# Kernel optimization log

Hardware: AMD Instinct MI355X
Metric: run time of the kernel (lower is better)

Reference implementation:

```python
import jax, jax.numpy as jnp
import numpy as np

HID = 512; NH = 8; HD = 64          # attention dims
SH = 8; SD = 32; SDIM = 256          # delta-state dims
NL = 6; FFN = 1536; VOC = 63
THETA = 500000.0; EPS = 1e-6


def rmsnorm(x, w, eps=EPS):
    xf = x.astype(jnp.float32)
    n = xf * jax.lax.rsqrt(jnp.mean(xf * xf, axis=-1, keepdims=True) + eps)
    return (n * w).astype(x.dtype)


def rotate_half(x):
    x1, x2 = jnp.split(x, 2, axis=-1)
    return jnp.concatenate([-x2, x1], axis=-1)


def delta_state(h, S0, Wk, Wv, Wq, Wbw, Wbb, Waw, Wab, Wout, nw, gw):
    # Gated delta-rule associative memory. h: (B,L,HID), S0: (B,SH,SD,SD)
    B, L, _ = h.shape
    k = (h @ Wk.T).reshape(B, L, SH, SD)
    v = (h @ Wv.T).reshape(B, L, SH, SD)
    q = (h @ Wq.T).reshape(B, L, SH, SD)
    beta = jax.nn.sigmoid(h @ Wbw.T + Wbb).reshape(B, L, SH, SD)
    alpha = jax.nn.sigmoid(h @ Waw.T + Wab).reshape(B, L, SH, SD)
    k = k / jnp.maximum(jnp.linalg.norm(k, axis=-1, keepdims=True), 1e-12)
    gate = h @ gw.T  # (B,L,SDIM)
    xs = tuple(jnp.moveaxis(a, 1, 0) for a in (k, v, q, beta, alpha))  # (L,B,SH,SD)

    def step(S, inp):
        k_t, v_t, q_t, b_t, a_t = inp
        S = S * a_t[..., None]                                  # decay rows
        pred = jnp.einsum('bhij,bhj->bhi', S, k_t)
        S = S + jnp.einsum('bhi,bhj->bhij', b_t * (v_t - pred), k_t)
        return S, jnp.einsum('bhij,bhj->bhi', S, q_t)

    S, reads = jax.lax.scan(step, S0, xs)
    ctx = jnp.moveaxis(reads, 0, 1).reshape(B, L, SDIM)
    ctx = rmsnorm(ctx, nw) * jax.nn.silu(gate)
    return ctx @ Wout.T, S


def attention(h, cos, sin, wq, wk, wv, wo):
    B, L, _ = h.shape
    q = (h @ wq.T).reshape(B, L, NH, HD).transpose(0, 2, 1, 3)
    k = (h @ wk.T).reshape(B, L, NH, HD).transpose(0, 2, 1, 3)
    v = (h @ wv.T).reshape(B, L, NH, HD).transpose(0, 2, 1, 3)
    c, s = cos[None, None], sin[None, None]
    q = q * c + rotate_half(q) * s
    k = k * c + rotate_half(k) * s
    scores = jnp.einsum('bhqd,bhkd->bhqk', q, k) / np.float32(np.sqrt(HD))
    mask = jnp.tril(jnp.ones((L, L), bool))
    scores = jnp.where(mask, scores, jnp.float32(-1e9))
    a = jax.nn.softmax(scores, axis=-1)
    o = jnp.einsum('bhqk,bhkd->bhqd', a, v).transpose(0, 2, 1, 3).reshape(B, L, HID)
    return o @ wo.T


def rope_tables(L, dtype):
    inv_freq = 1.0 / THETA ** (np.arange(0, HD, 2, dtype=np.float32) / HD)
    t = np.arange(L, dtype=np.float32)
    freqs = np.outer(t, inv_freq)
    emb = np.concatenate([freqs, freqs], axis=-1)
    return jnp.asarray(np.cos(emb), dtype), jnp.asarray(np.sin(emb), dtype)


def setup_inputs() -> dict:
    key = jax.random.key(0)
    ks = jax.random.split(key, 40)
    p = lambda i, shp: jax.random.normal(ks[i], shp, jnp.float32) * 0.02
    inp = {
        'input_ids': jax.random.randint(ks[0], (4, 1024), 0, VOC),
        'state': jnp.zeros((4, SH, SD, SD), jnp.float32),
        'embed': p(1, (VOC, HID)),
    }
    for j, pre in enumerate(['sr_', 'sw_']):
        b = 2 + j * 10
        inp[pre + 'Wk'] = p(b, (SDIM, HID)); inp[pre + 'Wv'] = p(b + 1, (SDIM, HID))
        inp[pre + 'Wq'] = p(b + 2, (SDIM, HID)); inp[pre + 'Wbw'] = p(b + 3, (SDIM, HID))
        inp[pre + 'Wbb'] = jnp.zeros((SDIM,), jnp.float32)
        inp[pre + 'Waw'] = p(b + 4, (SDIM, HID))
        inp[pre + 'Wab'] = jnp.full((SDIM,), 2.0, jnp.float32)
        inp[pre + 'Wout'] = p(b + 5, (HID, SDIM)); inp[pre + 'nw'] = jnp.ones((SDIM,), jnp.float32)
        inp[pre + 'gw'] = p(b + 6, (SDIM, HID))
    inp['ln1_w'] = jnp.ones((NL, HID), jnp.float32)
    inp['wq'] = p(25, (NL, HID, HID)); inp['wk'] = p(26, (NL, HID, HID))
    inp['wv'] = p(27, (NL, HID, HID)); inp['wo'] = p(28, (NL, HID, HID))
    inp['ln2_w'] = jnp.ones((NL, HID), jnp.float32)
    inp['w_gate'] = p(29, (NL, FFN, HID)); inp['w_up'] = p(30, (NL, FFN, HID))
    inp['w_down'] = p(31, (NL, HID, FFN))
    inp['final_norm_w'] = jnp.ones((HID,), jnp.float32)
    return inp


def reference(input_ids, state, embed,
              sr_Wk, sr_Wv, sr_Wq, sr_Wbw, sr_Wbb, sr_Waw, sr_Wab, sr_Wout, sr_nw, sr_gw,
              sw_Wk, sw_Wv, sw_Wq, sw_Wbw, sw_Wbb, sw_Waw, sw_Wab, sw_Wout, sw_nw, sw_gw,
              ln1_w, wq, wk, wv, wo, ln2_w, w_gate, w_up, w_down, final_norm_w):
    B, L = input_ids.shape
    h = embed[input_ids]
    cos, sin = rope_tables(L, h.dtype)
    read_out, S = delta_state(h, state, sr_Wk, sr_Wv, sr_Wq, sr_Wbw, sr_Wbb, sr_Waw, sr_Wab, sr_Wout, sr_nw, sr_gw)
    h = h + read_out
    for i in range(NL):
        a = attention(rmsnorm(h, ln1_w[i]), cos, sin, wq[i], wk[i], wv[i], wo[i])
        h = h + a
        x = rmsnorm(h, ln2_w[i])
        h = h + (jax.nn.silu(x @ w_gate[i].T) * (x @ w_up[i].T)) @ w_down[i].T
    write_out, S = delta_state(h, S, sw_Wk, sw_Wv, sw_Wq, sw_Wbw, sw_Wbb, sw_Waw, sw_Wab, sw_Wout, sw_nw, sw_gw)
    h = h + write_out
    h = rmsnorm(h, final_norm_w)
    logits = h @ embed.T  # tied embeddings
    return logits, S
```

## Files before the change

kernel.cpp:

```cpp
#include <hip/hip_runtime.h>
#include <hip/hip_bf16.h>
#include <math.h>


#define LSEQ 1024
#define BATCH 4
#define HIDDEN 512
#define NHEAD 8
#define HDIM 64
#define SHEAD 8
#define SDHD 32
#define SDIMM 256
#define FFND 1536
#define VOCN 63
#define ATTS 72

typedef __bf16 bf16;
typedef __attribute__((ext_vector_type(8))) __bf16 bf16x8;
typedef __attribute__((ext_vector_type(4))) float floatx4;

union BF4 { bf16 h[4]; short4 p; };

__device__ __forceinline__ void gload16(const void* g, const void* l) {
    __builtin_amdgcn_global_load_lds(
        (__attribute__((address_space(1))) unsigned int*)(uintptr_t)g,
        (__attribute__((address_space(3))) unsigned int*)(unsigned int)(uintptr_t)l,
        16, 0, 0);
}

__device__ __forceinline__ float sum8(float x) {
    x += __int_as_float(__builtin_amdgcn_mov_dpp(__float_as_int(x), 0xB1, 0xF, 0xF, true));
    x += __int_as_float(__builtin_amdgcn_mov_dpp(__float_as_int(x), 0x4E, 0xF, 0xF, true));
    x += __int_as_float(__builtin_amdgcn_mov_dpp(__float_as_int(x), 0x141, 0xF, 0xF, true));
    return x;
}

__device__ __forceinline__ int xcd_swz(int lin, int nwg) {
    int q = nwg >> 3, r = nwg & 7;
    int xcd = lin & 7, sub = lin >> 3;
    return (xcd < r ? xcd * (q + 1) : r * (q + 1) + (xcd - r) * q) + sub;
}

__global__ void rope_tables_k(float* __restrict__ cosT, float* __restrict__ sinT) {
    int idx = blockIdx.x * 256 + threadIdx.x;
    int l = idx >> 5, d = idx & 31;
    double ang = (double)l * pow(500000.0, -(double)(2 * d) / 64.0);
    cosT[idx] = (float)cos(ang);
    sinT[idx] = (float)sin(ang);
}

__global__ void embed_k(const int* __restrict__ ids, const float* __restrict__ emb,
                        float* __restrict__ h) {
    int tok = blockIdx.x;
    int id = ids[tok];
    ((float4*)(h + (size_t)tok * HIDDEN))[threadIdx.x] =
        ((const float4*)(emb + (size_t)id * HIDDEN))[threadIdx.x];
}

__global__ void cast_plain(const float* __restrict__ s, bf16* __restrict__ d, int n4) {
    int i = blockIdx.x * 256 + threadIdx.x;
    if (i >= n4) return;
    float4 v = ((const float4*)s)[i];
    BF4 u;
    u.h[0] = (bf16)v.x; u.h[1] = (bf16)v.y; u.h[2] = (bf16)v.z; u.h[3] = (bf16)v.w;
    ((short4*)d)[i] = u.p;
}

__global__ void cast6(const float* s0, const float* s1, const float* s2,
                      const float* s3, const float* s4, const float* s5,
                      bf16* __restrict__ d) {
    int i = blockIdx.x * 256 + threadIdx.x;
    if (i >= 196608) return;
    int which = i >> 15, loc = i & 32767;
    const float* s = which == 0 ? s0 : which == 1 ? s1 : which == 2 ? s2
                    : which == 3 ? s3 : which == 4 ? s4 : s5;
    float4 v = ((const float4*)s)[loc];
    BF4 u;
    u.h[0] = (bf16)v.x; u.h[1] = (bf16)v.y; u.h[2] = (bf16)v.z; u.h[3] = (bf16)v.w;
    ((short4*)d)[i] = u.p;
}

__global__ void cast_qkv(const float* __restrict__ q, const float* __restrict__ k,
                         const float* __restrict__ v, bf16* __restrict__ d) {
    int idx = blockIdx.x * 256 + threadIdx.x;
    if (idx >= 1179648) return;
    int which = idx / 393216;
    int rem = idx - which * 393216;
    const float* s = which == 0 ? q : which == 1 ? k : v;
    int layer = rem >> 16, rr = rem & 65535;
    int r = rr >> 7, c4 = rr & 127;
    float4 x = ((const float4*)s)[rem];
    BF4 u;
    u.h[0] = (bf16)x.x; u.h[1] = (bf16)x.y; u.h[2] = (bf16)x.z; u.h[3] = (bf16)x.w;
    ((short4*)d)[((size_t)layer * 1536 + which * 512 + r) * 128 + c4] = u.p;
}

__global__ void cast_gu(const float* __restrict__ g, const float* __restrict__ uu,
                        bf16* __restrict__ d) {
    int idx = blockIdx.x * 256 + threadIdx.x;
    if (idx >= 2359296) return;
    int which = idx / 1179648;
    int rem = idx - which * 1179648;
    const float* s = which == 0 ? g : uu;
    int layer = rem / 196608, rr = rem - layer * 196608;
    int r = rr >> 7, c4 = rr & 127;
    float4 x = ((const float4*)s)[rem];
    BF4 u;
    u.h[0] = (bf16)x.x; u.h[1] = (bf16)x.y; u.h[2] = (bf16)x.z; u.h[3] = (bf16)x.w;
    ((short4*)d)[((size_t)layer * 3072 + r * 2 + which) * 128 + c4] = u.p;
}

__global__ void cast_embed_pad(const float* __restrict__ s, bf16* __restrict__ d) {
    int i = blockIdx.x * 256 + threadIdx.x;
    int row = i >> 7, c4 = i & 127;
    BF4 u;
    if (row < VOCN) {
        float4 v = ((const float4*)s)[row * 128 + c4];
        u.h[0] = (bf16)v.x; u.h[1] = (bf16)v.y; u.h[2] = (bf16)v.z; u.h[3] = (bf16)v.w;
    } else {
        u.h[0] = (bf16)0.f; u.h[1] = (bf16)0.f; u.h[2] = (bf16)0.f; u.h[3] = (bf16)0.f;
    }
    ((short4*)d)[i] = u.p;
}

__global__ void rmsnorm512(const float* __restrict__ in, const float* __restrict__ w,
                           bf16* __restrict__ out) {
    int row = blockIdx.x, t = threadIdx.x;
    float4 x = ((const float4*)(in + (size_t)row * 512))[t];
    float s = x.x * x.x + x.y * x.y + x.z * x.z + x.w * x.w;
    for (int m = 1; m < 64; m <<= 1) s += __shfl_xor(s, m);
    __shared__ float red[2];
    if ((t & 63) == 0) red[t >> 6] = s;
    __syncthreads();
    float tot = red[0] + red[1];
    float r = rsqrtf(tot * (1.f / 512.f) + 1e-6f);
    float4 wv = ((const float4*)w)[t];
    BF4 u;
    u.h[0] = (bf16)(x.x * r * wv.x); u.h[1] = (bf16)(x.y * r * wv.y);
    u.h[2] = (bf16)(x.z * r * wv.z); u.h[3] = (bf16)(x.w * r * wv.w);
    ((short4*)(out + (size_t)row * 512))[t] = u.p;
}

template <int MODE>
__global__ __launch_bounds__(256) void gemm_bf16(const bf16* __restrict__ A,
                                                 const bf16* __restrict__ B,
                                                 float* __restrict__ C,
                                                 bf16* __restrict__ Cb,
                                                 const float* __restrict__ cosT,
                                                 const float* __restrict__ sinT,
                                                 bf16* __restrict__ Qb,
                                                 bf16* __restrict__ Kb,
                                                 bf16* __restrict__ Vtb,
                                                 int M, int N, int K, int Nreal) {
    __shared__ bf16 As[128 * 64];
    __shared__ bf16 Bs[128 * 64];
    const int tid = threadIdx.x;
    const int wave = tid >> 6, lane = tid & 63;
    const int nx = gridDim.x;
    const int wg = xcd_swz(blockIdx.y * nx + blockIdx.x, nx * gridDim.y);
    const int row0 = (wg / nx) * 128, col0 = (wg % nx) * 128;
    floatx4 acc[4][4];
#pragma unroll
    for (int i = 0; i < 4; ++i)
#pragma unroll
        for (int j = 0; j < 4; ++j) acc[i][j] = (floatx4){0.f, 0.f, 0.f, 0.f};
    const int m0 = (wave & 1) * 64, n0 = (wave >> 1) * 64;
    const int sr = tid >> 3;
    const int ske = ((tid & 7) ^ (sr & 7)) * 8;
    char* AsB = (char*)As;
    char* BsB = (char*)Bs;
    const int ldst = wave * 1024;
    const int ua0 = (((lane >> 4) + 0) ^ (lane & 7)) * 16;
    const int ua1 = (((lane >> 4) + 4) ^ (lane & 7)) * 16;

    for (int k0 = 0; k0 < K; k0 += 64) {
#pragma unroll
        for (int j = 0; j < 4; ++j) {
            gload16(A + (size_t)(row0 + j * 32 + sr) * K + ske + k0,
                    AsB + j * 4096 + ldst);
            gload16(B + (size_t)(col0 + j * 32 + sr) * K + ske + k0,
                    BsB + j * 4096 + ldst);
        }
        __syncthreads();
#pragma unroll
        for (int kk = 0; kk < 2; ++kk) {
            const int uu = kk ? ua1 : ua0;
            bf16x8 af[4], bfr[4];
#pragma unroll
            for (int mi = 0; mi < 4; ++mi)
                af[mi] = *(const bf16x8*)(AsB + (m0 + mi * 16 + (lane & 15)) * 128 + uu);
#pragma unroll
            for (int ni = 0; ni < 4; ++ni)
                bfr[ni] = *(const bf16x8*)(BsB + (n0 + ni * 16 + (lane & 15)) * 128 + uu);
#pragma unroll
            for (int mi = 0; mi < 4; ++mi)
#pragma unroll
                for (int ni = 0; ni < 4; ++ni)
                    acc[mi][ni] = __builtin_amdgcn_mfma_f32_16x16x32_bf16(af[mi], bfr[ni], acc[mi][ni], 0, 0, 0);
        }
        __syncthreads();
    }
    const int cr = (lane >> 4) * 4;
    const int cc = lane & 15;
    if (MODE == 5) {
        int segbase = col0 + n0;
        int seg = segbase >> 9;
        int head = (segbase >> 6) & 7;
        if (seg < 2) {
#pragma unroll
            for (int mi = 0; mi < 4; ++mi) {
#pragma unroll
                for (int r = 0; r < 4; ++r) {
                    int row = row0 + m0 + mi * 16 + cr + r;
                    int b = row >> 10, l = row & 1023;
                    size_t bh = (size_t)(b * 8 + head);
                    float x0 = acc[mi][0][r], x1 = acc[mi][1][r];
                    float x2 = acc[mi][2][r], x3 = acc[mi][3][r];
                    float c0 = cosT[l * 32 + cc], c1 = cosT[l * 32 + 16 + cc];
                    float s0 = sinT[l * 32 + cc], s1 = sinT[l * 32 + 16 + cc];
                    bf16* dst = (seg == 0 ? Qb : Kb) + bh * 65536 + l * 64;
                    dst[cc]      = (bf16)(x0 * c0 - x2 * s0);
                    dst[16 + cc] = (bf16)(x1 * c1 - x3 * s1);
                    dst[32 + cc] = (bf16)(x2 * c0 + x0 * s0);
                    dst[48 + cc] = (bf16)(x3 * c1 + x1 * s1);
                }
            }
        } else {
            char* T = (wave < 2) ? ((char*)As + wave * 8192)
                                 : ((char*)Bs + (wave - 2) * 8192);
            int lb = row0 + m0;
            int b = lb >> 10, l0 = lb & 1023;
            size_t bh = (size_t)(b * 8 + head);
            const int quad = lane >> 4;
            const int u = (quad >> 1);
            const int h = (quad & 1) * 8;
#pragma unroll
            for (int mi = 0; mi < 4; ++mi) {
#pragma unroll
                for (int ni = 0; ni < 4; ++ni) {
                    int d = ni * 16 + cc;
                    BF4 pk;
                    pk.h[0] = (bf16)acc[mi][ni][0];
                    pk.h[1] = (bf16)acc[mi][ni][1];
                    pk.h[2] = (bf16)acc[mi][ni][2];
                    pk.h[3] = (bf16)acc[mi][ni][3];
                    *(short4*)(T + d * 128 + ((mi * 2 + u) ^ (d & 7)) * 16 + h) = pk.p;
                }
            }
            int dl = lane >> 3, j = lane & 7;
#pragma unroll
            for (int i = 0; i < 8; ++i) {
                int d = i * 8 + dl;
                bf16x8 v = *(const bf16x8*)(T + d * 128 + ((j ^ dl) * 16));
                *(bf16x8*)(Vtb + bh * 65536 + (size_t)d * 1024 + l0 + j * 8) = v;
            }
        }
        return;
    }
#pragma unroll
    for (int mi = 0; mi < 4; ++mi) {
#pragma unroll
        for (int ni = 0; ni < 4; ++ni) {
#pragma unroll
            for (int r = 0; r < 4; ++r) {
                int row = row0 + m0 + mi * 16 + cr + r;
                int col = col0 + n0 + ni * 16 + cc;
                float v = acc[mi][ni][r];
                if (MODE == 4) {
                    float o = __shfl_xor(v, 1);
                    if (!(lane & 1)) {
                        float sg = v / (1.f + __expf(-v));
                        Cb[(size_t)row * Nreal + (col >> 1)] = (bf16)(sg * o);
                    }
                } else if (col < Nreal) {
                    size_t off = (size_t)row * Nreal + col;
                    if (MODE == 0) C[off] = v;
                }
            }
        }
    }
}

template <int MODE>
__global__ __launch_bounds__(256) void gemm64_bf16(const bf16* __restrict__ A,
                                                   const bf16* __restrict__ B,
                                                   float* __restrict__ C,
                                                   int M, int N, int K, int Nreal) {
    __shared__ bf16 As[2][64 * 64];
    __shared__ bf16 Bs[2][128 * 64];
    const int tid = threadIdx.x;
    const int wave = tid >> 6, lane = tid & 63;
    const int nx = gridDim.x;
    const int wg = xcd_swz(blockIdx.y * nx + blockIdx.x, nx * gridDim.y);
    const int row0 = (wg / nx) * 64, col0 = (wg % nx) * 128;
    floatx4 acc[2][4];
#pragma unroll
    for (int i = 0; i < 2; ++i)
#pragma unroll
        for (int j = 0; j < 4; ++j) acc[i][j] = (floatx4){0.f, 0.f, 0.f, 0.f};
    const int m0 = (wave & 1) * 32, n0 = (wave >> 1) * 64;
    const int sr = tid >> 3;
    const int ske = ((tid & 7) ^ (sr & 7)) * 8;
    const int ldst = wave * 1024;
    const int ua0 = (((lane >> 4) + 0) ^ (lane & 7)) * 16;
    const int ua1 = (((lane >> 4) + 4) ^ (lane & 7)) * 16;

    auto stage = [&](int k0, int buf) {
        char* AsB = (char*)As[buf];
        char* BsB = (char*)Bs[buf];
#pragma unroll
        for (int j = 0; j < 2; ++j)
            gload16(A + (size_t)(row0 + j * 32 + sr) * K + ske + k0,
                    AsB + j * 4096 + ldst);
#pragma unroll
        for (int j = 0; j < 4; ++j)
            gload16(B + (size_t)(col0 + j * 32 + sr) * K + ske + k0,
                    BsB + j * 4096 + ldst);
    };

    const int nk = K >> 6;
    stage(0, 0);
    __syncthreads();
    int cur = 0;
    for (int t = 0; t < nk; ++t, cur ^= 1) {
        if (t + 1 < nk) stage((t + 1) * 64, cur ^ 1);
        const char* AsB = (const char*)As[cur];
        const char* BsB = (const char*)Bs[cur];
#pragma unroll
        for (int kk = 0; kk < 2; ++kk) {
            const int uu = kk ? ua1 : ua0;
            bf16x8 af[2], bfr[4];
#pragma unroll
            for (int mi = 0; mi < 2; ++mi)
                af[mi] = *(const bf16x8*)(AsB + (m0 + mi * 16 + (lane & 15)) * 128 + uu);
#pragma unroll
            for (int ni = 0; ni < 4; ++ni)
                bfr[ni] = *(const bf16x8*)(BsB + (n0 + ni * 16 + (lane & 15)) * 128 + uu);
#pragma unroll
            for (int mi = 0; mi < 2; ++mi)
#pragma unroll
                for (int ni = 0; ni < 4; ++ni)
                    acc[mi][ni] = __builtin_amdgcn_mfma_f32_16x16x32_bf16(af[mi], bfr[ni], acc[mi][ni], 0, 0, 0);
        }
        __syncthreads();
    }
    const int cr = (lane >> 4) * 4;
    const int cc = lane & 15;
#pragma unroll
    for (int mi = 0; mi < 2; ++mi) {
#pragma unroll
        for (int ni = 0; ni < 4; ++ni) {
#pragma unroll
            for (int r = 0; r < 4; ++r) {
                int row = row0 + m0 + mi * 16 + cr + r;
                int col = col0 + n0 + ni * 16 + cc;
                if (col < Nreal) {
                    size_t off = (size_t)row * Nreal + col;
                    float v = acc[mi][ni][r];
                    if (MODE == 0) C[off] = v;
                    else C[off] += v;
                }
            }
        }
    }
}

__global__ __launch_bounds__(256) void attn_mfma(const bf16* __restrict__ Qb,
                                                 const bf16* __restrict__ Kb,
                                                 const bf16* __restrict__ Vtb,
                                                 bf16* __restrict__ O) {
    int qt = blockIdx.x, hh = blockIdx.y, b = blockIdx.z;
    int bh = b * 8 + hh;
    int q0 = qt * 64;
    const bf16* Qg = Qb + ((size_t)bh * 1024 + q0) * 64;
    const bf16* Kg = Kb + (size_t)bh * 1024 * 64;
    const bf16* Vg = Vtb + (size_t)bh * 64 * 1024;
    __shared__ bf16 Qs[64 * ATTS];
    __shared__ bf16 Ks[64 * ATTS];
    __shared__ bf16 Vs[64 * ATTS];
    __shared__ bf16 Ps[64 * ATTS];
    int tid = threadIdx.x, wave = tid >> 6, lane = tid & 63;
    int lr = lane & 15, quad = lane >> 4;

#pragma unroll
    for (int it = 0; it < 2; ++it) {
        int cidx = tid + it * 256;
        int row = cidx >> 3, ch = cidx & 7;
        *(bf16x8*)(Qs + row * ATTS + ch * 8) = *(const bf16x8*)(Qg + row * 64 + ch * 8);
    }
    float mrow[4], lrow[4];
    floatx4 Oacc[4];
#pragma unroll
    for (int r = 0; r < 4; ++r) { mrow[r] = -1e30f; lrow[r] = 0.f; }
#pragma unroll
    for (int d0 = 0; d0 < 4; ++d0) Oacc[d0] = (floatx4){0.f, 0.f, 0.f, 0.f};

    int ntiles = qt + 1;
    for (int t = 0; t < ntiles; ++t) {
        int kv0 = t * 64;
        __syncthreads();
#pragma unroll
        for (int it = 0; it < 2; ++it) {
            int cidx = tid + it * 256;
            int row = cidx >> 3, ch = cidx & 7;
            *(bf16x8*)(Ks + row * ATTS + ch * 8) =
                *(const bf16x8*)(Kg + (size_t)(kv0 + row) * 64 + ch * 8);
            *(bf16x8*)(Vs + row * ATTS + ch * 8) =
                *(const bf16x8*)(Vg + (size_t)row * 1024 + kv0 + ch * 8);
        }
        __syncthreads();
        bf16x8 aq[2];
#pragma unroll
        for (int kc = 0; kc < 2; ++kc)
            aq[kc] = *(const bf16x8*)(Qs + (wave * 16 + lr) * ATTS + kc * 32 + quad * 8);
        floatx4 sacc[4];
#pragma unroll
        for (int n0 = 0; n0 < 4; ++n0) {
            bf16x8 bk0 = *(const bf16x8*)(Ks + (n0 * 16 + lr) * ATTS + quad * 8);
            bf16x8 bk1 = *(const bf16x8*)(Ks + (n0 * 16 + lr) * ATTS + 32 + quad * 8);
            floatx4 z = (floatx4){0.f, 0.f, 0.f, 0.f};
            z = __builtin_amdgcn_mfma_f32_16x16x32_bf16(aq[0], bk0, z, 0, 0, 0);
            sacc[n0] = __builtin_amdgcn_mfma_f32_16x16x32_bf16(aq[1], bk1, z, 0, 0, 0);
        }
        float sv[4][4];
#pragma unroll
        for (int n0 = 0; n0 < 4; ++n0)
#pragma unroll
            for (int r = 0; r < 4; ++r) sv[n0][r] = sacc[n0][r] * 0.125f;
        if (t == ntiles - 1) {
#pragma unroll
            for (int n0 = 0; n0 < 4; ++n0)
#pragma unroll
                for (int r = 0; r < 4; ++r)
                    if (n0 * 16 + lr > wave * 16 + quad * 4 + r) sv[n0][r] = -1e30f;
        }
        float al[4];
#pragma unroll
        for (int r = 0; r < 4; ++r) {
            float tm = fmaxf(fmaxf(sv[0][r], sv[1][r]), fmaxf(sv[2][r], sv[3][r]));
            tm = fmaxf(tm, __shfl_xor(tm, 1));
            tm = fmaxf(tm, __shfl_xor(tm, 2));
            tm = fmaxf(tm, __shfl_xor(tm, 4));
            tm = fmaxf(tm, __shfl_xor(tm, 8));
            float mn = fmaxf(mrow[r], tm);
            al[r] = __expf(mrow[r] - mn);
            mrow[r] = mn;
        }
        float rs[4];
#pragma unroll
        for (int r = 0; r < 4; ++r) rs[r] = 0.f;
#pragma unroll
        for (int n0 = 0; n0 < 4; ++n0)
#pragma unroll
            for (int r = 0; r < 4; ++r) {
                float p = __expf(sv[n0][r] - mrow[r]);
                sv[n0][r] = p;
                rs[r] += p;
            }
#pragma unroll
        for (int r = 0; r < 4; ++r) {
            float t2 = rs[r];
            t2 += __shfl_xor(t2, 1);
            t2 += __shfl_xor(t2, 2);
            t2 += __shfl_xor(t2, 4);
            t2 += __shfl_xor(t2, 8);
            lrow[r] = lrow[r] * al[r] + t2;
        }
#pragma unroll
        for (int d0 = 0; d0 < 4; ++d0)
#pragma unroll
            for (int r = 0; r < 4; ++r) Oacc[d0][r] *= al[r];
#pragma unroll
        for (int n0 = 0; n0 < 4; ++n0)
#pragma unroll
            for (int r = 0; r < 4; ++r)
                Ps[(wave * 16 + quad * 4 + r) * ATTS + n0 * 16 + lr] = (bf16)sv[n0][r];
        bf16x8 ap[2];
#pragma unroll
        for (int kc = 0; kc < 2; ++kc)
            ap[kc] = *(const bf16x8*)(Ps + (wave * 16 + lr) * ATTS + kc * 32 + quad * 8);
#pragma unroll
        for (int d0 = 0; d0 < 4; ++d0) {
            bf16x8 bv0 = *(const bf16x8*)(Vs + (d0 * 16 + lr) * ATTS + quad * 8);
            bf16x8 bv1 = *(const bf16x8*)(Vs + (d0 * 16 + lr) * ATTS + 32 + quad * 8);
            Oacc[d0] = __builtin_amdgcn_mfma_f32_16x16x32_bf16(ap[0], bv0, Oacc[d0], 0, 0, 0);
            Oacc[d0] = __builtin_amdgcn_mfma_f32_16x16x32_bf16(ap[1], bv1, Oacc[d0], 0, 0, 0);
        }
    }
    float inv[4];
#pragma unroll
    for (int r = 0; r < 4; ++r) inv[r] = 1.f / lrow[r];
#pragma unroll
    for (int d0 = 0; d0 < 4; ++d0)
#pragma unroll
        for (int r = 0; r < 4; ++r) {
            int row = b * 1024 + q0 + wave * 16 + quad * 4 + r;
            int col = hh * 64 + d0 * 16 + lr;
            O[(size_t)row * 512 + col] = (bf16)(Oacc[d0][r] * inv[r]);
        }
}

__global__ __launch_bounds__(512, 2) void delta_scan(
    const float* __restrict__ P, const float* __restrict__ S_in,
    const float* __restrict__ bbias, const float* __restrict__ abias,
    float* __restrict__ S_out, float* __restrict__ ctx) {
    int bh = blockIdx.x;
    int b = bh >> 3, hh = bh & 7;
    int tid = threadIdx.x;
    int role = tid >> 8;
    int htid = tid & 255;
    int lane = htid & 63;
    int wv = htid >> 6;
    int ri = wv * 8 + (lane >> 3);
    int c = lane & 7;
    bool cz = (c == 0);
    __shared__ __align__(16) float ks[2][66][36], qs[2][66][36], vs[2][66][36],
                                   bs[2][66][36], as_[2][66][36];
    __shared__ __align__(16) float cpair[2][33][4];
    __shared__ __align__(16) float cs[64][32];
    float4 S = *(const float4*)(S_in + ((size_t)bh * 32 + ri) * 32 + c * 4);

    int sc4 = htid & 7, sr0 = htid >> 3;
    float4 bB = *(const float4*)(bbias + hh * 32 + sc4 * 4);
    float4 bA = *(const float4*)(abias + hh * 32 + sc4 * 4);

    struct Pair {
        float4 k1, k2, q1, q2;
        float a1, a2, b1, b2, bv1, bv2;
        float c12, cq11, cq12, cq22;
    };

    auto dot4 = [](float4 s, float4 k) {
        return fmaf(s.w, k.w, fmaf(s.z, k.z, fmaf(s.y, k.y, s.x * k.x)));
    };

    auto stage_chunk = [&](int c0, int buf) {
        float (*ksH)[36] = ks[buf];
        float (*qsH)[36] = qs[buf];
        float (*vsH)[36] = vs[buf];
        float (*bsH)[36] = bs[buf];
        float (*asH)[36] = as_[buf];
        float (*cpH)[4]  = cpair[buf];
        const float* Pb = P + ((size_t)(b * 1024 + c0) * 1536) + hh * 32 + sc4 * 4;
#pragma unroll
        for (int it = 0; it < 2; ++it) {
            int tok = sr0 + it * 32;
            const float* pg = Pb + (size_t)tok * 1536;
            float4 kv = *(const float4*)(pg);
            float4 vv = *(const float4*)(pg + 256);
            float4 qv = *(const float4*)(pg + 512);
            float4 bv = *(const float4*)(pg + 768);
            float4 av = *(const float4*)(pg + 1024);
            float ss = kv.x * kv.x + kv.y * kv.y + kv.z * kv.z + kv.w * kv.w;
            ss = sum8(ss);
            float rn = 1.f / fmaxf(sqrtf(ss), 1e-12f);
            kv.x *= rn; kv.y *= rn; kv.z *= rn; kv.w *= rn;
            float4 bo, ao;
            bo.x = 1.f / (1.f + __expf(-(bv.x + bB.x)));
            bo.y = 1.f / (1.f + __expf(-(bv.y + bB.y)));
            bo.z = 1.f / (1.f + __expf(-(bv.z + bB.z)));
            bo.w = 1.f / (1.f + __expf(-(bv.w + bB.w)));
            ao.x = 1.f / (1.f + __expf(-(av.x + bA.x)));
            ao.y = 1.f / (1.f + __expf(-(av.y + bA.y)));
            ao.z = 1.f / (1.f + __expf(-(av.z + bA.z)));
            ao.w = 1.f / (1.f + __expf(-(av.w + bA.w)));
            float4 vo;
            vo.x = bo.x * vv.x; vo.y = bo.y * vv.y;
            vo.z = bo.z * vv.z; vo.w = bo.w * vv.w;
            float kq = sum8(kv.x * qv.x + kv.y * qv.y + kv.z * qv.z + kv.w * qv.w);
            float4 ko, qo;
            ko.x = __shfl_xor(kv.x, 8); ko.y = __shfl_xor(kv.y, 8);
            ko.z = __shfl_xor(kv.z, 8); ko.w = __shfl_xor(kv.w, 8);
            qo.x = __shfl_xor(qv.x, 8); qo.y = __shfl_xor(qv.y, 8);
            qo.z = __shfl_xor(qv.z, 8); qo.w = __shfl_xor(qv.w, 8);
            float ckk = sum8(kv.x * ko.x + kv.y * ko.y + kv.z * ko.z + kv.w * ko.w);
            float ckq = sum8(kv.x * qo.x + kv.y * qo.y + kv.z * qo.z + kv.w * qo.w);
            *(float4*)&ksH[tok][sc4 * 4] = kv;
            *(float4*)&vsH[tok][sc4 * 4] = vo;
            *(float4*)&qsH[tok][sc4 * 4] = qv;
            *(float4*)&bsH[tok][sc4 * 4] = bo;
            *(float4*)&asH[tok][sc4 * 4] = ao;
            if ((htid & 7) == 0) {
                int pairi = tok >> 1;
                if (!(tok & 1)) {
                    cpH[pairi][0] = ckk;
                    cpH[pairi][1] = kq;
                    cpH[pairi][2] = ckq;
                } else {
                    cpH[pairi][3] = kq;
                }
            }
        }
    };

    auto scan_chunk = [&](int c0, int buf) {
        float (*ksH)[36] = ks[buf];
        float (*qsH)[36] = qs[buf];
        float (*vsH)[36] = vs[buf];
        float (*bsH)[36] = bs[buf];
        float (*asH)[36] = as_[buf];
        float (*cpH)[4]  = cpair[buf];
        auto loadp = [&](int t, Pair& Pr) {
            Pr.k1 = *(const float4*)&ksH[2 * t][c * 4];
            Pr.k2 = *(const float4*)&ksH[2 * t + 1][c * 4];
            Pr.q1 = *(const float4*)&qsH[2 * t][c * 4];
            Pr.q2 = *(const float4*)&qsH[2 * t + 1][c * 4];
            Pr.a1 = asH[2 * t][ri];  Pr.a2 = asH[2 * t + 1][ri];
            Pr.b1 = bsH[2 * t][ri];  Pr.b2 = bsH[2 * t + 1][ri];
            Pr.bv1 = vsH[2 * t][ri]; Pr.bv2 = vsH[2 * t + 1][ri];
            float4 cp = *(const float4*)&cpH[t][0];
            Pr.c12 = cp.x; Pr.cq11 = cp.y; Pr.cq12 = cp.z; Pr.cq22 = cp.w;
        };
        auto stepp = [&](const Pair& Pr, int t) {
            float d1  = sum8(dot4(S, Pr.k1));
            float d2  = sum8(dot4(S, Pr.k2));
            float dq1 = sum8(dot4(S, Pr.q1));
            float dq2 = sum8(dot4(S, Pr.q2));
            float u1 = fmaf(-(Pr.b1 * Pr.a1), d1, Pr.bv1);
            float au1 = Pr.a2 * u1;
            float A = Pr.a1 * Pr.a2;
            float pred2 = fmaf(au1, Pr.c12, A * d2);
            float u2 = fmaf(-Pr.b2, pred2, Pr.bv2);
            S.x = fmaf(u2, Pr.k2.x, fmaf(au1, Pr.k1.x, A * S.x));
            S.y = fmaf(u2, Pr.k2.y, fmaf(au1, Pr.k1.y, A * S.y));
            S.z = fmaf(u2, Pr.k2.z, fmaf(au1, Pr.k1.z, A * S.z));
            S.w = fmaf(u2, Pr.k2.w, fmaf(au1, Pr.k1.w, A * S.w));
            if (cz) {
                cs[2 * t][ri]     = fmaf(u1, Pr.cq11, Pr.a1 * dq1);
                cs[2 * t + 1][ri] = fmaf(u2, Pr.cq22, fmaf(au1, Pr.cq12, A * dq2));
            }
        };
        Pair PA, PB;
        loadp(0, PA);
        for (int t = 0; t < 32; t += 2) {
            loadp(t + 1, PB);
            stepp(PA, t);
            loadp(t + 2, PA);
            stepp(PB, t + 1);
        }
        int gbase = b * 1024 + c0;
#pragma unroll
        for (int it = 0; it < 2; ++it) {
            int e = lane + it * 64;
            int t = e >> 1, j4 = wv * 2 + (e & 1);
            float4 val = *(const float4*)&cs[t][j4 * 4];
            *(float4*)(ctx + (size_t)(gbase + t) * 256 + hh * 32 + j4 * 4) = val;
        }
    };

    if (role == 1) stage_chunk(0, 0);
    __syncthreads();
    for (int ch = 0; ch < 16; ++ch) {
        if (role == 1) {
            if (ch + 1 < 16) stage_chunk((ch + 1) * 64, (ch + 1) & 1);
        } else {
            scan_chunk(ch * 64, ch & 1);
        }
        __syncthreads();
    }
    if (role == 0)
        *(float4*)(S_out + ((size_t)bh * 32 + ri) * 32 + c * 4) = S;
}

__global__ void ctx_post(const float* __restrict__ ctx, const float* __restrict__ P,
                         const float* __restrict__ nw, bf16* __restrict__ out) {
    int row = blockIdx.x, t = threadIdx.x;
    float4 x = ((const float4*)(ctx + (size_t)row * SDIMM))[t];
    float s = x.x * x.x + x.y * x.y + x.z * x.z + x.w * x.w;
    for (int m = 1; m < 64; m <<= 1) s += __shfl_xor(s, m);
    float r = rsqrtf(s * (1.f / 256.f) + 1e-6f);
    float4 n = ((const float4*)nw)[t];
    float4 g = ((const float4*)(P + (size_t)row * 1536 + 1280))[t];
    BF4 u;
    u.h[0] = (bf16)(x.x * r * n.x * (g.x / (1.f + __expf(-g.x))));
    u.h[1] = (bf16)(x.y * r * n.y * (g.y / (1.f + __expf(-g.y))));
    u.h[2] = (bf16)(x.z * r * n.z * (g.z / (1.f + __expf(-g.z))));
    u.h[3] = (bf16)(x.w * r * n.w * (g.w / (1.f + __expf(-g.w))));
    ((short4*)(out + (size_t)row * SDIMM))[t] = u.p;
}

extern "C" void kernel_launch(void* const* d_in, const int* in_sizes, int n_in,
                              void* d_out, int out_size, void* d_ws, size_t ws_size,
                              hipStream_t stream) {
    (void)in_sizes; (void)n_in; (void)out_size; (void)ws_size;
    const int* ids = (const int*)d_in[0];
    const float* state = (const float*)d_in[1];
    const float* embedw = (const float*)d_in[2];
    auto F = [&](int i) { return (const float*)d_in[i]; };

    char* wsb = (char*)d_ws;
    const size_t MB = 1048576;
    float* H    = (float*)(wsb);
    bf16*  XNbf = (bf16*)(wsb + 8 * MB);
    float* ctxf = (float*)(wsb + 8 * MB);
    bf16*  Hbf  = (bf16*)(wsb + 12 * MB);
    bf16*  ctxb = (bf16*)(wsb + 12 * MB);
    float* P    = (float*)(wsb + 16 * MB);
    bf16*  Obf  = (bf16*)(wsb + 40 * MB);
    bf16*  Qbuf = (bf16*)(wsb + 44 * MB);
    bf16*  Kbuf = (bf16*)(wsb + 48 * MB);
    bf16*  Vtb  = (bf16*)(wsb + 52 * MB);
    bf16*  A1b  = (bf16*)(wsb + 44 * MB);
    float* cosT = (float*)(wsb + 58 * MB);
    float* sinT = cosT + 32768;
    float* Sbuf = sinT + 32768;
    char*  wbase = wsb + 59 * MB;
    bf16* wqkv  = (bf16*)(wbase);
    bf16* wob   = (bf16*)(wbase + 9437184);
    bf16* wgu   = (bf16*)(wbase + 12582912);
    bf16* wdnb  = (bf16*)(wbase + 31457280);
    bf16* wdR   = (bf16*)(wbase + 40894464);
    bf16* woutR = (bf16*)(wbase + 42467328);
    bf16* wdW   = (bf16*)(wbase + 42729472);
    bf16* woutW = (bf16*)(wbase + 44302336);
    bf16* embp  = (bf16*)(wbase + 44564480);

    float* out = (float*)d_out;
    float* logits = out;
    float* Sout = out + 4096 * VOCN;

    auto G0 = [&](const bf16* A, const bf16* B, float* C, int M, int N, int K, int Nreal) {
        gemm_bf16<0><<<dim3(N / 128, M / 128), 256, 0, stream>>>(
            A, B, C, nullptr, nullptr, nullptr, nullptr, nullptr, nullptr, M, N, K, Nreal);
    };
    auto G4 = [&](const bf16* A, const bf16* B, bf16* Cb, int M, int N, int K, int Nreal) {
        gemm_bf16<4><<<dim3(N / 128, M / 128), 256, 0, stream>>>(
            A, B, nullptr, Cb, nullptr, nullptr, nullptr, nullptr, nullptr, M, N, K, Nreal);
    };
    auto G5 = [&](const bf16* A, const bf16* B, int M, int N, int K) {
        gemm_bf16<5><<<dim3(N / 128, M / 128), 256, 0, stream>>>(
            A, B, nullptr, nullptr, cosT, sinT, Qbuf, Kbuf, Vtb, M, N, K, N);
    };
    auto G1s = [&](const bf16* A, const bf16* B, float* C, int M, int N, int K) {
        gemm64_bf16<1><<<dim3(N / 128, M / 64), 256, 0, stream>>>(A, B, C, M, N, K, N);
    };
    auto G0s = [&](const bf16* A, const bf16* B, float* C, int M, int N, int K, int Nreal) {
        gemm64_bf16<0><<<dim3(N / 128, M / 64), 256, 0, stream>>>(A, B, C, M, N, K, Nreal);
    };
    auto CP = [&](const float* s, bf16* d, int n4) {
        cast_plain<<<(n4 + 255) / 256, 256, 0, stream>>>(s, d, n4);
    };

    cast_qkv<<<4608, 256, 0, stream>>>(F(24), F(25), F(26), wqkv);
    CP(F(27), wob, 393216);
    cast_gu<<<9216, 256, 0, stream>>>(F(29), F(30), wgu);
    CP(F(31), wdnb, 1179648);
    cast6<<<768, 256, 0, stream>>>(F(3), F(4), F(5), F(6), F(8), F(12), wdR);
    CP(F(10), woutR, 32768);
    cast6<<<768, 256, 0, stream>>>(F(13), F(14), F(15), F(16), F(18), F(22), wdW);
    CP(F(20), woutW, 32768);
    cast_embed_pad<<<64, 256, 0, stream>>>(embedw, embp);

    rope_tables_k<<<128, 256, 0, stream>>>(cosT, sinT);
    embed_k<<<4096, 128, 0, stream>>>(ids, embedw, H);

    CP(H, Hbf, 524288);
    G0(Hbf, wdR, P, 4096, 1536, 512, 1536);
    delta_scan<<<32, 512, 0, stream>>>(P, state, F(7), F(9), Sbuf, ctxf);
    ctx_post<<<4096, 64, 0, stream>>>(ctxf, P, F(11), ctxb);
    G1s(ctxb, woutR, H, 4096, 512, 256);

    for (int i = 0; i < 6; ++i) {
        rmsnorm512<<<4096, 128, 0, stream>>>(H, F(23) + (size_t)i * 512, XNbf);
        G5(XNbf, wqkv + (size_t)i * 1536 * 512, 4096, 1536, 512);
        attn_mfma<<<dim3(16, 8, 4), 256, 0, stream>>>(Qbuf, Kbuf, Vtb, Obf);
        G1s(Obf, wob + (size_t)i * 512 * 512, H, 4096, 512, 512);
        rmsnorm512<<<4096, 128, 0, stream>>>(H, F(28) + (size_t)i * 512, XNbf);
        G4(XNbf, wgu + (size_t)i * 3072 * 512, A1b, 4096, 3072, 512, 1536);
        G1s(A1b, wdnb + (size_t)i * 512 * 1536, H, 4096, 512, 1536);
    }

    CP(H, Hbf, 524288);
    G0(Hbf, wdW, P, 4096, 1536, 512, 1536);
    delta_scan<<<32, 512, 0, stream>>>(P, Sbuf, F(17), F(19), Sout, ctxf);
    ctx_post<<<4096, 64, 0, stream>>>(ctxf, P, F(21), ctxb);
    G1s(ctxb, woutW, H, 4096, 512, 256);

    rmsnorm512<<<4096, 128, 0, stream>>>(H, F(32), XNbf);
    G0s(XNbf, embp, logits, 4096, 128, 512, VOCN);
}
```

Baseline: 1.188 ms.

## Merge setup cast kernels into one launch; reorder attention tiles and raise MFMA priority

Eleven separate weight-cast, rope-table and embedding kernels are folded into one cast_all kernel, with each block range dispatching to one sub-task. This removes per-launch overhead and the gaps between launches. The attention kernel also reverses the query-tile order for half the batches, to even out causal work across the grid. It wraps its MFMA sections in s_setprio to favour matrix issue. The merged kernel's branch-by-block-index layout has to match the old index math exactly.

```diff
diff --git a/kernel.cpp b/kernel.cpp
--- a/kernel.cpp
+++ b/kernel.cpp
@@ -41,22 +41,6 @@
     return (xcd < r ? xcd * (q + 1) : r * (q + 1) + (xcd - r) * q) + sub;
 }
 
-__global__ void rope_tables_k(float* __restrict__ cosT, float* __restrict__ sinT) {
-    int idx = blockIdx.x * 256 + threadIdx.x;
-    int l = idx >> 5, d = idx & 31;
-    double ang = (double)l * pow(500000.0, -(double)(2 * d) / 64.0);
-    cosT[idx] = (float)cos(ang);
-    sinT[idx] = (float)sin(ang);
-}
-
-__global__ void embed_k(const int* __restrict__ ids, const float* __restrict__ emb,
-                        float* __restrict__ h) {
-    int tok = blockIdx.x;
-    int id = ids[tok];
-    ((float4*)(h + (size_t)tok * HIDDEN))[threadIdx.x] =
-        ((const float4*)(emb + (size_t)id * HIDDEN))[threadIdx.x];
-}
-
 __global__ void cast_plain(const float* __restrict__ s, bf16* __restrict__ d, int n4) {
     int i = blockIdx.x * 256 + threadIdx.x;
     if (i >= n4) return;
@@ -66,61 +50,89 @@
     ((short4*)d)[i] = u.p;
 }
 
-__global__ void cast6(const float* s0, const float* s1, const float* s2,
-                      const float* s3, const float* s4, const float* s5,
-                      bf16* __restrict__ d) {
-    int i = blockIdx.x * 256 + threadIdx.x;
-    if (i >= 196608) return;
-    int which = i >> 15, loc = i & 32767;
-    const float* s = which == 0 ? s0 : which == 1 ? s1 : which == 2 ? s2
-                    : which == 3 ? s3 : which == 4 ? s4 : s5;
-    float4 v = ((const float4*)s)[loc];
+struct CastArgs {
+    const float *wq, *wk, *wv, *wob, *wg, *wu, *wdn;
+    const float *r0, *r1, *r2, *r3, *r4, *r5, *woutR;
+    const float *w0, *w1, *w2, *w3, *w4, *w5, *woutW;
+    const float *emb; const int *ids;
+    bf16 *wqkvD, *wobD, *wguD, *wdnbD, *wdRD, *woutRD, *wdWD, *woutWD, *embpD;
+    float *cosT, *sinT, *H;
+};
+
+__device__ __forceinline__ void cast4(const float* s, bf16* d, int i) {
+    float4 v = ((const float4*)s)[i];
     BF4 u;
     u.h[0] = (bf16)v.x; u.h[1] = (bf16)v.y; u.h[2] = (bf16)v.z; u.h[3] = (bf16)v.w;
     ((short4*)d)[i] = u.p;
 }
 
-__global__ void cast_qkv(const float* __restrict__ q, const float* __restrict__ k,
-                         const float* __restrict__ v, bf16* __restrict__ d) {
-    int idx = blockIdx.x * 256 + threadIdx.x;
-    if (idx >= 1179648) return;
-    int which = idx / 393216;
-    int rem = idx - which * 393216;
-    const float* s = which == 0 ? q : which == 1 ? k : v;
-    int layer = rem >> 16, rr = rem & 65535;
-    int r = rr >> 7, c4 = rr & 127;
-    float4 x = ((const float4*)s)[rem];
-    BF4 u;
-    u.h[0] = (bf16)x.x; u.h[1] = (bf16)x.y; u.h[2] = (bf16)x.z; u.h[3] = (bf16)x.w;
-    ((short4*)d)[((size_t)layer * 1536 + which * 512 + r) * 128 + c4] = u.p;
-}
-
-__global__ void cast_gu(const float* __restrict__ g, const float* __restrict__ uu,
-                        bf16* __restrict__ d) {
-    int idx = blockIdx.x * 256 + threadIdx.x;
-    if (idx >= 2359296) return;
-    int which = idx / 1179648;
-    int rem = idx - which * 1179648;
-    const float* s = which == 0 ? g : uu;
-    int layer = rem / 196608, rr = rem - layer * 196608;
-    int r = rr >> 7, c4 = rr & 127;
-    float4 x = ((const float4*)s)[rem];
-    BF4 u;
-    u.h[0] = (bf16)x.x; u.h[1] = (bf16)x.y; u.h[2] = (bf16)x.z; u.h[3] = (bf16)x.w;
-    ((short4*)d)[((size_t)layer * 3072 + r * 2 + which) * 128 + c4] = u.p;
-}
-
-__global__ void cast_embed_pad(const float* __restrict__ s, bf16* __restrict__ d) {
-    int i = blockIdx.x * 256 + threadIdx.x;
-    int row = i >> 7, c4 = i & 127;
-    BF4 u;
-    if (row < VOCN) {
-        float4 v = ((const float4*)s)[row * 128 + c4];
-        u.h[0] = (bf16)v.x; u.h[1] = (bf16)v.y; u.h[2] = (bf16)v.z; u.h[3] = (bf16)v.w;
+__global__ void cast_all(CastArgs a) {
+    int bx = blockIdx.x, tid = threadIdx.x;
+    if (bx < 4608) {
+        int idx = bx * 256 + tid;
+        int which = idx / 393216;
+        int rem = idx - which * 393216;
+        const float* s = which == 0 ? a.wq : which == 1 ? a.wk : a.wv;
+        int layer = rem >> 16, rr = rem & 65535;
+        int r = rr >> 7, c4 = rr & 127;
+        float4 x = ((const float4*)s)[rem];
+        BF4 u;
+        u.h[0] = (bf16)x.x; u.h[1] = (bf16)x.y; u.h[2] = (bf16)x.z; u.h[3] = (bf16)x.w;
+        ((short4*)a.wqkvD)[((size_t)layer * 1536 + which * 512 + r) * 128 + c4] = u.p;
+    } else if (bx < 6144) {
+        cast4(a.wob, a.wobD, (bx - 4608) * 256 + tid);
+    } else if (bx < 15360) {
+        int idx = (bx - 6144) * 256 + tid;
+        int which = idx / 1179648;
+        int rem = idx - which * 1179648;
+        const float* s = which == 0 ? a.wg : a.wu;
+        int layer = rem / 196608, rr = rem - layer * 196608;
+        int r = rr >> 7, c4 = rr & 127;
+        float4 x = ((const float4*)s)[rem];
+        BF4 u;
+        u.h[0] = (bf16)x.x; u.h[1] = (bf16)x.y; u.h[2] = (bf16)x.z; u.h[3] = (bf16)x.w;
+        ((short4*)a.wguD)[((size_t)layer * 3072 + r * 2 + which) * 128 + c4] = u.p;
+    } else if (bx < 19968) {
+        cast4(a.wdn, a.wdnbD, (bx - 15360) * 256 + tid);
+    } else if (bx < 20736) {
+        int i = (bx - 19968) * 256 + tid;
+        int which = i >> 15, loc = i & 32767;
+        const float* s = which == 0 ? a.r0 : which == 1 ? a.r1 : which == 2 ? a.r2
+                        : which == 3 ? a.r3 : which == 4 ? a.r4 : a.r5;
+        cast4(s, a.wdRD + (size_t)which * 131072, loc);
+    } else if (bx < 20864) {
+        cast4(a.woutR, a.woutRD, (bx - 20736) * 256 + tid);
+    } else if (bx < 21632) {
+        int i = (bx - 20864) * 256 + tid;
+        int which = i >> 15, loc = i & 32767;
+        const float* s = which == 0 ? a.w0 : which == 1 ? a.w1 : which == 2 ? a.w2
+                        : which == 3 ? a.w3 : which == 4 ? a.w4 : a.w5;
+        cast4(s, a.wdWD + (size_t)which * 131072, loc);
+    } else if (bx < 21760) {
+        cast4(a.woutW, a.woutWD, (bx - 21632) * 256 + tid);
+    } else if (bx < 21824) {
+        int i = (bx - 21760) * 256 + tid;
+        int row = i >> 7, c4 = i & 127;
+        BF4 u;
+        if (row < VOCN) {
+            float4 v = ((const float4*)a.emb)[row * 128 + c4];
+            u.h[0] = (bf16)v.x; u.h[1] = (bf16)v.y; u.h[2] = (bf16)v.z; u.h[3] = (bf16)v.w;
+        } else {
+            u.h[0] = (bf16)0.f; u.h[1] = (bf16)0.f; u.h[2] = (bf16)0.f; u.h[3] = (bf16)0.f;
+        }
+        ((short4*)a.embpD)[i] = u.p;
+    } else if (bx < 21952) {
+        int idx = (bx - 21824) * 256 + tid;
+        int l = idx >> 5, d = idx & 31;
+        double ang = (double)l * pow(500000.0, -(double)(2 * d) / 64.0);
+        a.cosT[idx] = (float)cos(ang);
+        a.sinT[idx] = (float)sin(ang);
     } else {
-        u.h[0] = (bf16)0.f; u.h[1] = (bf16)0.f; u.h[2] = (bf16)0.f; u.h[3] = (bf16)0.f;
-    }
-    ((short4*)d)[i] = u.p;
+        int tok = (bx - 21952) * 2 + (tid >> 7);
+        int id = a.ids[tok];
+        ((float4*)(a.H + (size_t)tok * HIDDEN))[tid & 127] =
+            ((const float4*)(a.emb + (size_t)id * HIDDEN))[tid & 127];
+    }
 }
 
 __global__ void rmsnorm512(const float* __restrict__ in, const float* __restrict__ w,
@@ -370,6 +382,7 @@
                                                  const bf16* __restrict__ Vtb,
                                                  bf16* __restrict__ O) {
     int qt = blockIdx.x, hh = blockIdx.y, b = blockIdx.z;
+    if (b & 2) qt = gridDim.x - 1 - qt;
     int bh = b * 8 + hh;
     int q0 = qt * 64;
     const bf16* Qg = Qb + ((size_t)bh * 1024 + q0) * 64;
@@ -414,6 +427,7 @@
         for (int kc = 0; kc < 2; ++kc)
             aq[kc] = *(const bf16x8*)(Qs + (wave * 16 + lr) * ATTS + kc * 32 + quad * 8);
         floatx4 sacc[4];
+        __builtin_amdgcn_s_setprio(1);
 #pragma unroll
         for (int n0 = 0; n0 < 4; ++n0) {
             bf16x8 bk0 = *(const bf16x8*)(Ks + (n0 * 16 + lr) * ATTS + quad * 8);
@@ -422,6 +436,7 @@
             z = __builtin_amdgcn_mfma_f32_16x16x32_bf16(aq[0], bk0, z, 0, 0, 0);
             sacc[n0] = __builtin_amdgcn_mfma_f32_16x16x32_bf16(aq[1], bk1, z, 0, 0, 0);
         }
+        __builtin_amdgcn_s_setprio(0);
         float sv[4][4];
 #pragma unroll
         for (int n0 = 0; n0 < 4; ++n0)
@@ -479,6 +494,7 @@
 #pragma unroll
         for (int kc = 0; kc < 2; ++kc)
             ap[kc] = *(const bf16x8*)(Ps + (wave * 16 + lr) * ATTS + kc * 32 + quad * 8);
+        __builtin_amdgcn_s_setprio(1);
 #pragma unroll
         for (int d0 = 0; d0 < 4; ++d0) {
             bf16x8 bv0 = *(const bf16x8*)(Vs + (d0 * 16 + lr) * ATTS + quad * 8);
@@ -486,6 +502,7 @@
             Oacc[d0] = __builtin_amdgcn_mfma_f32_16x16x32_bf16(ap[0], bv0, Oacc[d0], 0, 0, 0);
             Oacc[d0] = __builtin_amdgcn_mfma_f32_16x16x32_bf16(ap[1], bv1, Oacc[d0], 0, 0, 0);
         }
+        __builtin_amdgcn_s_setprio(0);
     }
     float inv[4];
 #pragma unroll
@@ -741,18 +758,18 @@
         cast_plain<<<(n4 + 255) / 256, 256, 0, stream>>>(s, d, n4);
     };
 
-    cast_qkv<<<4608, 256, 0, stream>>>(F(24), F(25), F(26), wqkv);
-    CP(F(27), wob, 393216);
-    cast_gu<<<9216, 256, 0, stream>>>(F(29), F(30), wgu);
-    CP(F(31), wdnb, 1179648);
-    cast6<<<768, 256, 0, stream>>>(F(3), F(4), F(5), F(6), F(8), F(12), wdR);
-    CP(F(10), woutR, 32768);
-    cast6<<<768, 256, 0, stream>>>(F(13), F(14), F(15), F(16), F(18), F(22), wdW);
-    CP(F(20), woutW, 32768);
-    cast_embed_pad<<<64, 256, 0, stream>>>(embedw, embp);
-
-    rope_tables_k<<<128, 256, 0, stream>>>(cosT, sinT);
-    embed_k<<<4096, 128, 0, stream>>>(ids, embedw, H);
+    CastArgs ca;
+    ca.wq = F(24); ca.wk = F(25); ca.wv = F(26); ca.wob = F(27);
+    ca.wg = F(29); ca.wu = F(30); ca.wdn = F(31);
+    ca.r0 = F(3); ca.r1 = F(4); ca.r2 = F(5); ca.r3 = F(6); ca.r4 = F(8); ca.r5 = F(12);
+    ca.woutR = F(10);
+    ca.w0 = F(13); ca.w1 = F(14); ca.w2 = F(15); ca.w3 = F(16); ca.w4 = F(18); ca.w5 = F(22);
+    ca.woutW = F(20);
+    ca.emb = embedw; ca.ids = ids;
+    ca.wqkvD = wqkv; ca.wobD = wob; ca.wguD = wgu; ca.wdnbD = wdnb;
+    ca.wdRD = wdR; ca.woutRD = woutR; ca.wdWD = wdW; ca.woutWD = woutW;
+    ca.embpD = embp; ca.cosT = cosT; ca.sinT = sinT; ca.H = H;
+    cast_all<<<24000, 256, 0, stream>>>(ca);
 
     CP(H, Hbf, 524288);
     G0(Hbf, wdR, P, 4096, 1536, 512, 1536);
```

Result: faster. 1.121 ms (-5.7%).
